# Performance work log

Hardware: AMD Instinct MI355X
Metric: run time of the kernel (lower is better)

The kernel has to match this reference:

```python
import jax, jax.numpy as jnp
import numpy as np
import math

S, B, H, NH = 2048, 1, 4096, 32
HD = H // NH          # 128 head dim
ROT = HD // 2         # 64 rotary dim per half (position_encoding_2d)


def _rotary_tables(seq_len):
    inv_freq = 1.0 / (10000.0 ** (jnp.arange(0, ROT, 2, dtype=jnp.float32) / ROT))  # [ROT/2]
    t = jnp.arange(seq_len, dtype=jnp.float32)
    freqs = jnp.einsum('i,j->ij', t, inv_freq)          # [S, ROT/2]
    emb = jnp.concatenate([freqs, freqs], axis=-1)       # [S, ROT]
    return jnp.cos(emb), jnp.sin(emb)


def _rotate_half(x):
    half = x.shape[-1] // 2
    return jnp.concatenate([-x[..., half:], x[..., :half]], axis=-1)


def _apply_rotary(q, k, cos, sin, pos):
    # q,k: [s,b,nh,ROT]; pos: [s,b]
    c = cos[pos][:, :, None, :]   # [s,b,1,ROT]
    s_ = sin[pos][:, :, None, :]
    return q * c + _rotate_half(q) * s_, k * c + _rotate_half(k) * s_


def reference(hidden_states, position_ids, attention_mask, layer_id, w_qkv, b_qkv, w_dense, b_dense):
    s, b, _ = hidden_states.shape
    # fused QKV projection (Linear: x @ W.T + b)
    qkv = jnp.einsum('sbh,oh->sbo', hidden_states, w_qkv) + b_qkv     # [s,b,3H]
    qkv = qkv.reshape(s, b, NH, 3 * HD)
    q, k, v = jnp.split(qkv, 3, axis=-1)                               # each [s,b,nh,HD]
    # 2D rotary: split head dim in two halves, rotate with pos / block pos ids
    cos, sin = _rotary_tables(s)
    pos = position_ids[:, 0, :].T        # [s,b]
    blk = position_ids[:, 1, :].T        # [s,b]
    q1, q2 = jnp.split(q, 2, axis=-1)
    k1, k2 = jnp.split(k, 2, axis=-1)
    q1, k1 = _apply_rotary(q1, k1, cos, sin, pos)
    q2, k2 = _apply_rotary(q2, k2, cos, sin, blk)
    q = jnp.concatenate([q1, q2], axis=-1)
    k = jnp.concatenate([k1, k2], axis=-1)
    # layer-id-dependent scaling (GLM numerics): q scaled down by coeff, logits scaled back up
    coeff = float(layer_id + 1)
    q = q / (math.sqrt(HD) * coeff)
    scores = jnp.einsum('sbnd,tbnd->bnst', q, k)                       # [b,nh,s,s]
    scores = jnp.where(attention_mask, jnp.asarray(-10000.0, scores.dtype), scores)
    probs = jax.nn.softmax(scores.astype(jnp.float32) * coeff, axis=-1).astype(scores.dtype)
    ctx = jnp.einsum('bnst,tbnd->sbnd', probs, v).reshape(s, b, H)     # [s,b,H]
    return jnp.einsum('sbh,oh->sbo', ctx, w_dense) + b_dense


def setup_inputs() -> dict:
    key = jax.random.key(0)
    k1, k2, k3, k4, k5, k6 = jax.random.split(key, 6)
    init = 0.02
    hidden_states = jax.random.normal(k1, (S, B, H), dtype=jnp.float32)
    # GLM-style 2D position ids: [B, 2, S] (row 0: positions, row 1: block positions)
    pos = jnp.broadcast_to(jnp.arange(S, dtype=jnp.int64), (B, S))
    blk = jnp.broadcast_to(jnp.arange(S, dtype=jnp.int64), (B, S))
    position_ids = jnp.stack([pos, blk], axis=1)                        # [B,2,S]
    # causal mask: True = masked (future positions)
    causal = jnp.triu(jnp.ones((S, S), dtype=bool), k=1)
    attention_mask = jnp.broadcast_to(causal[None, None], (B, 1, S, S))
    return {
        'hidden_states': hidden_states,
        'position_ids': position_ids,
        'attention_mask': attention_mask,
        'layer_id': 5,
        'w_qkv': jax.random.normal(k2, (3 * H, H), dtype=jnp.float32) * init,
        'b_qkv': jax.random.normal(k3, (3 * H,), dtype=jnp.float32) * init,
        'w_dense': jax.random.normal(k4, (H, H), dtype=jnp.float32) * init,
        'b_dense': jax.random.normal(k5, (H,), dtype=jnp.float32) * init,
    }
```

## Files before the change

### kernel.cpp

```cpp
#include <hip/hip_runtime.h>
#include <math.h>
#include <stdint.h>

constexpr int S  = 2048;
constexpr int H  = 4096;
constexpr int NH = 32;
constexpr int HD = 128;
constexpr int H3 = 3 * H;

typedef unsigned short u16;
typedef __bf16 bf16x8 __attribute__((ext_vector_type(8)));
typedef float  f32x4  __attribute__((ext_vector_type(4)));
typedef unsigned short us8 __attribute__((ext_vector_type(8)));

__device__ __forceinline__ u16 f2bf(float f) {
  uint32_t u = __float_as_uint(f);
  uint32_t r = (u + 0x7fff + ((u >> 16) & 1)) >> 16;
  return (u16)r;
}
__device__ __forceinline__ float bf2f(u16 u) {
  return __uint_as_float((uint32_t)u << 16);
}

__device__ __forceinline__ void load_lds16(const void* g, void* l) {
  __builtin_amdgcn_global_load_lds(
      (__attribute__((address_space(1))) void*)(uintptr_t)g,
      (__attribute__((address_space(3))) void*)l,
      16, 0, 0);
}

#define SBAR0 __builtin_amdgcn_sched_barrier(0)

__global__ __launch_bounds__(256)
void cast_all(const float* __restrict__ w_qkv, const float* __restrict__ hidden,
              const float* __restrict__ w_dense, u16* __restrict__ wq,
              u16* __restrict__ hb, u16* __restrict__ wd) {
  constexpr int NQ  = H3 * H / 4;
  constexpr int NHd = S * H / 4;
  constexpr int ND  = H * H / 4;
  constexpr int NT  = NQ + NHd + ND;
  for (int i = blockIdx.x * 256 + threadIdx.x; i < NT; i += gridDim.x * 256) {
    const float4* src;
    ushort4* dst;
    int j = i;
    if (j < NQ)            { src = (const float4*)w_qkv;  dst = (ushort4*)wq; }
    else if (j < NQ + NHd) { j -= NQ; src = (const float4*)hidden; dst = (ushort4*)hb; }
    else                   { j -= NQ + NHd; src = (const float4*)w_dense; dst = (ushort4*)wd; }
    float4 v = src[j];
    ushort4 o;
    o.x = f2bf(v.x); o.y = f2bf(v.y); o.z = f2bf(v.z); o.w = f2bf(v.w);
    dst[j] = o;
  }
}

template<int STRIDE, int OUT_BF16>
__global__ __launch_bounds__(512, 2)
void gemm256(const u16* __restrict__ A, const u16* __restrict__ W,
             const float* __restrict__ bias, void* __restrict__ Cout) {
  constexpr int K   = 4096;
  constexpr int NT  = K / 64;
  constexpr int NTM = 8;
  constexpr int TB  = 65536;
  __shared__ __attribute__((aligned(16))) unsigned char lds[2 * TB];
  const int tid = threadIdx.x, wave = tid >> 6, lane = tid & 63;
  const int l15 = lane & 15, l4 = lane >> 4;
  const int wr = wave >> 2, wc = wave & 3;

  const int nwg = gridDim.x, bid = blockIdx.x;
  const int cpx = nwg >> 3;
  const int swz = (bid & 7) * cpx + (bid >> 3);
  const int bx = swz / NTM, by = swz - bx * NTM;
  const int bm = by * 256, bn = bx * 256;

  const int srow = lane >> 3;
  const int sck  = ((lane & 7) ^ srow) * 8;
  const u16* Abase = A + (size_t)(bm + srow) * K + sck;
  const u16* Wbase = W + (size_t)(bn + srow) * K + sck;

  auto stageU = [&](int tt, int u) {
    const int b = tt & 1;
    if (u < 4) {
      const int rb = u * 64 + wave * 8;
      load_lds16(Abase + (size_t)rb * K + tt * 64, &lds[b * TB + rb * 128]);
    } else {
      const int rb = (u - 4) * 64 + wave * 8;
      load_lds16(Wbase + (size_t)rb * K + tt * 64,
                 &lds[b * TB + 32768 + rb * 128]);
    }
  };

  f32x4 acc[8][4];
#pragma unroll
  for (int i = 0; i < 8; ++i)
#pragma unroll
    for (int j = 0; j < 4; ++j) acc[i][j] = (f32x4)0.f;

#pragma unroll
  for (int u = 0; u < 8; ++u) stageU(0, u);
#pragma unroll
  for (int u = 0; u < 8; ++u) stageU(1, u);
  asm volatile("s_waitcnt vmcnt(8)" ::: "memory");
  SBAR0;
  __builtin_amdgcn_s_barrier();

  const int arow = wr * 128 + l15;
  const int brow = wc * 64 + l15;
  const int ckx  = l15 & 7;

  bf16x8 af[4][2], bfA[2][2], bfB[2][2];

  for (int t = 0; t < NT; ++t) {
    const int b0 = (t & 1) * TB;
    const bool st = (t + 2 < NT);
#pragma unroll
    for (int mi = 0; mi < 4; ++mi)
#pragma unroll
      for (int ks = 0; ks < 2; ++ks)
        af[mi][ks] = *(const bf16x8*)&lds[b0 + (arow + mi * 16) * 128 +
                                          (((ks * 4 + l4) ^ ckx) * 16)];
#pragma unroll
    for (int ni = 0; ni < 2; ++ni)
#pragma unroll
      for (int ks = 0; ks < 2; ++ks)
        bfA[ni][ks] = *(const bf16x8*)&lds[b0 + 32768 + (brow + ni * 16) * 128 +
                                           (((ks * 4 + l4) ^ ckx) * 16)];
    SBAR0; __builtin_amdgcn_s_barrier();
    asm volatile("s_waitcnt lgkmcnt(0)" ::: "memory");
    SBAR0;
    __builtin_amdgcn_s_setprio(1);
#pragma unroll
    for (int ks = 0; ks < 2; ++ks)
#pragma unroll
      for (int mi = 0; mi < 4; ++mi)
#pragma unroll
        for (int ni = 0; ni < 2; ++ni)
          acc[mi][ni] = __builtin_amdgcn_mfma_f32_16x16x32_bf16(af[mi][ks], bfA[ni][ks], acc[mi][ni], 0, 0, 0);
    __builtin_amdgcn_s_setprio(0);
    SBAR0; __builtin_amdgcn_s_barrier();
#pragma unroll
    for (int ni = 0; ni < 2; ++ni)
#pragma unroll
      for (int ks = 0; ks < 2; ++ks)
        bfB[ni][ks] = *(const bf16x8*)&lds[b0 + 32768 + (brow + (ni + 2) * 16) * 128 +
                                           (((ks * 4 + l4) ^ ckx) * 16)];
    if (st) { stageU(t + 2, 0); stageU(t + 2, 2); }
    SBAR0; __builtin_amdgcn_s_barrier();
    asm volatile("s_waitcnt lgkmcnt(0)" ::: "memory");
    SBAR0;
    __builtin_amdgcn_s_setprio(1);
#pragma unroll
    for (int ks = 0; ks < 2; ++ks)
#pragma unroll
      for (int mi = 0; mi < 4; ++mi)
#pragma unroll
        for (int ni = 0; ni < 2; ++ni)
          acc[mi][ni + 2] = __builtin_amdgcn_mfma_f32_16x16x32_bf16(af[mi][ks], bfB[ni][ks], acc[mi][ni + 2], 0, 0, 0);
    __builtin_amdgcn_s_setprio(0);
    SBAR0; __builtin_amdgcn_s_barrier();
#pragma unroll
    for (int mi = 0; mi < 4; ++mi)
#pragma unroll
      for (int ks = 0; ks < 2; ++ks)
        af[mi][ks] = *(const bf16x8*)&lds[b0 + (arow + (mi + 4) * 16) * 128 +
                                          (((ks * 4 + l4) ^ ckx) * 16)];
    if (st) { stageU(t + 2, 4); stageU(t + 2, 5); }
    SBAR0; __builtin_amdgcn_s_barrier();
    asm volatile("s_waitcnt lgkmcnt(0)" ::: "memory");
    SBAR0;
    __builtin_amdgcn_s_setprio(1);
#pragma unroll
    for (int ks = 0; ks < 2; ++ks)
#pragma unroll
      for (int mi = 0; mi < 4; ++mi)
#pragma unroll
        for (int ni = 0; ni < 2; ++ni)
          acc[mi + 4][ni] = __builtin_amdgcn_mfma_f32_16x16x32_bf16(af[mi][ks], bfA[ni][ks], acc[mi + 4][ni], 0, 0, 0);
    __builtin_amdgcn_s_setprio(0);
    SBAR0; __builtin_amdgcn_s_barrier();
    if (st) { stageU(t + 2, 1); stageU(t + 2, 3); stageU(t + 2, 6); stageU(t + 2, 7); }
    SBAR0;
    __builtin_amdgcn_s_setprio(1);
#pragma unroll
    for (int ks = 0; ks < 2; ++ks)
#pragma unroll
      for (int mi = 0; mi < 4; ++mi)
#pragma unroll
        for (int ni = 0; ni < 2; ++ni)
          acc[mi + 4][ni + 2] = __builtin_amdgcn_mfma_f32_16x16x32_bf16(af[mi][ks], bfB[ni][ks], acc[mi + 4][ni + 2], 0, 0, 0);
    __builtin_amdgcn_s_setprio(0);
    if (t < NT - 2)       asm volatile("s_waitcnt vmcnt(8)" ::: "memory");
    else if (t == NT - 2) asm volatile("s_waitcnt vmcnt(0)" ::: "memory");
    SBAR0;
    if (t < NT - 1) __builtin_amdgcn_s_barrier();
  }

#pragma unroll
  for (int ni = 0; ni < 4; ++ni) {
    const int col = bn + wc * 64 + ni * 16 + l15;
    const float bv = bias[col];
#pragma unroll
    for (int mi = 0; mi < 8; ++mi) {
#pragma unroll
      for (int r = 0; r < 4; ++r) {
        const int row = bm + wr * 128 + mi * 16 + l4 * 4 + r;
        const float v = acc[mi][ni][r] + bv;
        if (OUT_BF16) ((u16*)Cout)[(size_t)row * STRIDE + col] = f2bf(v);
        else          ((float*)Cout)[(size_t)row * STRIDE + col] = v;
      }
    }
  }
}

template<int STRIDE, int OUT_BF16>
__global__ __launch_bounds__(512, 2)
void gemm8p(const u16* __restrict__ A, const u16* __restrict__ W,
            const float* __restrict__ bias, void* __restrict__ Cout) {
  constexpr int K  = 4096;
  constexpr int NT = K / 64;
  constexpr int NTM = 16;
  constexpr int TB = 49152;
  __shared__ __attribute__((aligned(16))) unsigned char lds[3 * TB];
  const int tid = threadIdx.x, wave = tid >> 6, lane = tid & 63;
  const int l15 = lane & 15, l4 = lane >> 4;
  const int wr = wave >> 2, wc = wave & 3;

  const int nwg = gridDim.x, bid = blockIdx.x;
  const int cpx = nwg >> 3;
  const int swz = (bid & 7) * cpx + (bid >> 3);
  const int bx = swz / NTM, by = swz - bx * NTM;
  const int bm = by * 128, bn = bx * 256;

  const int srow = lane >> 3;
  const int sck  = ((lane & 7) ^ srow) * 8;
  const u16* Abase = A + (size_t)(bm + srow) * K + sck;
  const u16* Wbase = W + (size_t)(bn + srow) * K + sck;

  auto stageA = [&](int tt, int b) {
#pragma unroll
    for (int j = 0; j < 2; ++j) {
      const int rb = j * 64 + wave * 8;
      load_lds16(Abase + (size_t)rb * K + tt * 64, &lds[b * TB + rb * 128]);
    }
  };
  auto stageB = [&](int tt, int b, int u) {
#pragma unroll
    for (int j = 0; j < 2; ++j) {
      const int rb = u * 128 + j * 64 + wave * 8;
      load_lds16(Wbase + (size_t)rb * K + tt * 64,
                 &lds[b * TB + 16384 + rb * 128]);
    }
  };

  f32x4 acc[4][4];
#pragma unroll
  for (int i = 0; i < 4; ++i)
#pragma unroll
    for (int j = 0; j < 4; ++j) acc[i][j] = (f32x4)0.f;

  stageA(0, 0); stageB(0, 0, 0); stageB(0, 0, 1);
  stageA(1, 1); stageB(1, 1, 0); stageB(1, 1, 1);
  asm volatile("s_waitcnt vmcnt(6)" ::: "memory");
  SBAR0;
  __builtin_amdgcn_s_barrier();

  const int arow = wr * 64 + l15;
  const int brow = wc * 64 + l15;
  const int ckx  = l15 & 7;

  bf16x8 af[4][2], bf[4][2];

  int br = 0, bs = 2;
  for (int t = 0; t < NT; ++t) {
    const int b0 = br * TB;
#pragma unroll
    for (int mi = 0; mi < 2; ++mi)
#pragma unroll
      for (int ks = 0; ks < 2; ++ks)
        af[mi][ks] = *(const bf16x8*)&lds[b0 + (arow + mi * 16) * 128 +
                                          (((ks * 4 + l4) ^ ckx) * 16)];
#pragma unroll
    for (int ni = 0; ni < 2; ++ni)
#pragma unroll
      for (int ks = 0; ks < 2; ++ks)
        bf[ni][ks] = *(const bf16x8*)&lds[b0 + 16384 + (brow + ni * 16) * 128 +
                                          (((ks * 4 + l4) ^ ckx) * 16)];
    if (t < NT - 2) stageA(t + 2, bs);
    SBAR0; __builtin_amdgcn_s_barrier();
    asm volatile("s_waitcnt lgkmcnt(0)" ::: "memory");
    SBAR0;
    __builtin_amdgcn_s_setprio(1);
#pragma unroll
    for (int ks = 0; ks < 2; ++ks)
#pragma unroll
      for (int mi = 0; mi < 2; ++mi)
#pragma unroll
        for (int ni = 0; ni < 2; ++ni)
          acc[mi][ni] = __builtin_amdgcn_mfma_f32_16x16x32_bf16(af[mi][ks], bf[ni][ks], acc[mi][ni], 0, 0, 0);
    __builtin_amdgcn_s_setprio(0);
    SBAR0; __builtin_amdgcn_s_barrier();
#pragma unroll
    for (int ni = 2; ni < 4; ++ni)
#pragma unroll
      for (int ks = 0; ks < 2; ++ks)
        bf[ni][ks] = *(const bf16x8*)&lds[b0 + 16384 + (brow + ni * 16) * 128 +
                                          (((ks * 4 + l4) ^ ckx) * 16)];
    if (t < NT - 2) stageB(t + 2, bs, 0);
    SBAR0; __builtin_amdgcn_s_barrier();
    asm volatile("s_waitcnt lgkmcnt(0)" ::: "memory");
    SBAR0;
    __builtin_amdgcn_s_setprio(1);
#pragma unroll
    for (int ks = 0; ks < 2; ++ks)
#pragma unroll
      for (int mi = 0; mi < 2; ++mi)
#pragma unroll
        for (int ni = 2; ni < 4; ++ni)
          acc[mi][ni] = __builtin_amdgcn_mfma_f32_16x16x32_bf16(af[mi][ks], bf[ni][ks], acc[mi][ni], 0, 0, 0);
    __builtin_amdgcn_s_setprio(0);
    SBAR0; __builtin_amdgcn_s_barrier();
#pragma unroll
    for (int mi = 2; mi < 4; ++mi)
#pragma unroll
      for (int ks = 0; ks < 2; ++ks)
        af[mi][ks] = *(const bf16x8*)&lds[b0 + (arow + mi * 16) * 128 +
                                          (((ks * 4 + l4) ^ ckx) * 16)];
    if (t < NT - 2) stageB(t + 2, bs, 1);
    SBAR0; __builtin_amdgcn_s_barrier();
    asm volatile("s_waitcnt lgkmcnt(0)" ::: "memory");
    SBAR0;
    __builtin_amdgcn_s_setprio(1);
#pragma unroll
    for (int ks = 0; ks < 2; ++ks)
#pragma unroll
      for (int mi = 2; mi < 4; ++mi)
#pragma unroll
        for (int ni = 0; ni < 2; ++ni)
          acc[mi][ni] = __builtin_amdgcn_mfma_f32_16x16x32_bf16(af[mi][ks], bf[ni][ks], acc[mi][ni], 0, 0, 0);
    __builtin_amdgcn_s_setprio(0);
    SBAR0; __builtin_amdgcn_s_barrier();
    __builtin_amdgcn_s_setprio(1);
#pragma unroll
    for (int ks = 0; ks < 2; ++ks)
#pragma unroll
      for (int mi = 2; mi < 4; ++mi)
#pragma unroll
        for (int ni = 2; ni < 4; ++ni)
          acc[mi][ni] = __builtin_amdgcn_mfma_f32_16x16x32_bf16(af[mi][ks], bf[ni][ks], acc[mi][ni], 0, 0, 0);
    __builtin_amdgcn_s_setprio(0);
    if (t < NT - 1) {
      if (t < NT - 2) asm volatile("s_waitcnt vmcnt(6)" ::: "memory");
      else            asm volatile("s_waitcnt vmcnt(0)" ::: "memory");
      SBAR0;
      __builtin_amdgcn_s_barrier();
    }
    br = (br == 2) ? 0 : br + 1;
    bs = (bs == 2) ? 0 : bs + 1;
  }

#pragma unroll
  for (int ni = 0; ni < 4; ++ni) {
    const int col = bn + wc * 64 + ni * 16 + l15;
    const float bv = bias[col];
#pragma unroll
    for (int mi = 0; mi < 4; ++mi) {
#pragma unroll
      for (int r = 0; r < 4; ++r) {
        const int row = bm + wr * 64 + mi * 16 + l4 * 4 + r;
        const float v = acc[mi][ni][r] + bv;
        if (OUT_BF16) ((u16*)Cout)[(size_t)row * STRIDE + col] = f2bf(v);
        else          ((float*)Cout)[(size_t)row * STRIDE + col] = v;
      }
    }
  }
}

__global__ __launch_bounds__(256)
void rotary_fused(const u16* __restrict__ qkv,
                  u16* __restrict__ Qb, u16* __restrict__ Kb,
                  u16* __restrict__ Vt) {
  __shared__ u16 vt[64][136];
  __shared__ float2 cs_tab[64][32];
  const int s0 = blockIdx.x * 64, h = blockIdx.y;
  const int tid = threadIdx.x;

  for (int idx = tid; idx < 2048; idx += 256) {
    const int r = idx >> 5, j = idx & 31;
    const float invf = exp2f(-(float)j * (13.287712379549449f / 32.f));
    float sn, c;
    sincosf((float)(s0 + r) * invf, &sn, &c);
    cs_tab[r][j] = make_float2(c, sn);
  }
  for (int idx = tid; idx < 1024; idx += 256) {
    const int r = idx >> 4, ck = idx & 15;
    us8 v = *(const us8*)(qkv + (size_t)(s0 + r) * H3 + h * 384 + 256 + ck * 8);
    *(us8*)&vt[r][ck * 8] = v;
  }
  __syncthreads();

  for (int idx = tid; idx < 2048; idx += 256) {
    const int r  = idx >> 5;
    const int sub = idx & 31;
    const int tq = sub >> 4;
    const int ck = sub & 15;
    const int s = s0 + r;
    const u16* base = qkv + (size_t)s * H3 + h * 384 + tq * 128;
    us8 v = *(const us8*)(base + ck * 8);
    us8 p = *(const us8*)(base + ((ck * 8) ^ 32));
    const int d0 = ck * 8;
    const float sign = ((d0 & 63) < 32) ? -1.f : 1.f;
    const float sc = tq ? 1.f : 0.12751721769218683f;
    us8 o;
#pragma unroll
    for (int e = 0; e < 8; ++e) {
      const float2 cs = cs_tab[r][(d0 + e) & 31];
      o[e] = f2bf((bf2f(v[e]) * cs.x + sign * bf2f(p[e]) * cs.y) * sc);
    }
    *(us8*)((tq ? Kb : Qb) + ((size_t)h * S + s) * HD + d0) = o;
  }
  for (int idx = tid; idx < 1024; idx += 256) {
    const int d = idx >> 3, c8 = idx & 7;
    us8 o;
#pragma unroll
    for (int e = 0; e < 8; ++e) o[e] = vt[c8 * 8 + e][d];
    *(us8*)(Vt + ((size_t)h * HD + d) * S + s0 + c8 * 8) = o;
  }
}

__global__ __launch_bounds__(256)
void attn(const u16* __restrict__ Qb, const u16* __restrict__ Kb,
          const u16* __restrict__ Vt, u16* __restrict__ ctx) {
  __shared__ __attribute__((aligned(16))) unsigned char sK[2][64 * 256];
  __shared__ __attribute__((aligned(16))) unsigned char sV[2][128 * 128];
  __shared__ __attribute__((aligned(16))) unsigned char sP[4][16 * 128];
  const int bid = blockIdx.x;
  const int ixd = bid >> 3;
  const int h   = (bid & 7) * 4 + (ixd >> 5);
  const int qb  = 31 - (ixd & 31);
  const int tid = threadIdx.x, wave = tid >> 6, lane = tid & 63;
  const int l15 = lane & 15, l4 = lane >> 4;
  const int qw0 = qb * 64 + wave * 16;

  auto stage = [&](int it) {
    const int t0 = it * 64, b = it & 1;
#pragma unroll
    for (int c = 0; c < 4; ++c) {
      const int rbase = c * 16 + wave * 4;
      const int rr = rbase + (lane >> 4);
      const int p = lane & 15;
      load_lds16(Kb + ((size_t)h * S + t0 + rr) * HD + ((p ^ (rr & 15)) * 8),
                 &sK[b][rbase * 256]);
    }
#pragma unroll
    for (int c = 0; c < 4; ++c) {
      const int rbase = c * 32 + wave * 8;
      const int rr = rbase + (lane >> 3);
      const int p = lane & 7;
      load_lds16(Vt + ((size_t)h * HD + rr) * S + t0 + ((p ^ (rr & 7)) * 8),
                 &sV[b][rbase * 128]);
    }
  };

  bf16x8 qf[4];
  {
    const u16* qrow = Qb + ((size_t)h * S + qw0 + l15) * HD;
#pragma unroll
    for (int ks = 0; ks < 4; ++ks)
      qf[ks] = *(const bf16x8*)(qrow + ks * 32 + l4 * 8);
  }

  f32x4 of[8];
#pragma unroll
  for (int i = 0; i < 8; ++i) of[i] = (f32x4)0.f;
  float mrun[4] = {-1e30f, -1e30f, -1e30f, -1e30f};
  float lrun[4] = {0.f, 0.f, 0.f, 0.f};

  const int nt = qb + 1;
  stage(0);
  for (int it = 0; it < nt; ++it) {
    const int t0 = it * 64, b = it & 1;
    if (it + 1 < nt) {
      stage(it + 1);
      asm volatile("s_waitcnt vmcnt(8)" ::: "memory");
    } else {
      asm volatile("s_waitcnt vmcnt(0)" ::: "memory");
    }
    SBAR0;
    __builtin_amdgcn_s_barrier();
    SBAR0;

    f32x4 sc[4];
#pragma unroll
    for (int nf = 0; nf < 4; ++nf) sc[nf] = (f32x4)0.f;
#pragma unroll
    for (int nf = 0; nf < 4; ++nf) {
      const int trow = nf * 16 + l15;
#pragma unroll
      for (int ks = 0; ks < 4; ++ks) {
        const int chunk = ks * 4 + l4;
        bf16x8 kf = *(const bf16x8*)&sK[b][trow * 256 + ((chunk ^ (trow & 15)) * 16)];
        sc[nf] = __builtin_amdgcn_mfma_f32_16x16x32_bf16(qf[ks], kf, sc[nf], 0, 0, 0);
      }
    }

    if (it == qb) {
#pragma unroll
      for (int nf = 0; nf < 4; ++nf) {
        const int tg = t0 + nf * 16 + l15;
#pragma unroll
        for (int r = 0; r < 4; ++r) {
          const int sg = qw0 + l4 * 4 + r;
          if (tg > sg) sc[nf][r] = -1e30f;
        }
      }
    }

    f32x4 vm = sc[0];
#pragma unroll
    for (int nf = 1; nf < 4; ++nf)
#pragma unroll
      for (int r = 0; r < 4; ++r) vm[r] = fmaxf(vm[r], sc[nf][r]);
#pragma unroll
    for (int m = 1; m <= 8; m <<= 1)
#pragma unroll
      for (int r = 0; r < 4; ++r) vm[r] = fmaxf(vm[r], __shfl_xor(vm[r], m, 64));

    bool need = false;
#pragma unroll
    for (int r = 0; r < 4; ++r) need = need || (vm[r] > mrun[r] + 8.f);
    if (__builtin_amdgcn_ballot_w64(need)) {
#pragma unroll
      for (int r = 0; r < 4; ++r) {
        const float nm = fmaxf(mrun[r], vm[r]);
        const float scale = exp2f(mrun[r] - nm);
        mrun[r] = nm;
        lrun[r] *= scale;
#pragma unroll
        for (int i = 0; i < 8; ++i) of[i][r] *= scale;
      }
    }

    f32x4 rs = (f32x4)0.f;
#pragma unroll
    for (int nf = 0; nf < 4; ++nf) {
#pragma unroll
      for (int r = 0; r < 4; ++r) {
        const float p = exp2f(sc[nf][r] - mrun[r]);
        rs[r] += p;
        const int row = l4 * 4 + r;
        const int t = nf * 16 + l15;
        const int chunk = t >> 3;
        *(u16*)&sP[wave][row * 128 + ((chunk ^ (row & 7)) * 16) + (t & 7) * 2] = f2bf(p);
      }
    }
#pragma unroll
    for (int m = 1; m <= 8; m <<= 1)
#pragma unroll
      for (int r = 0; r < 4; ++r) rs[r] += __shfl_xor(rs[r], m, 64);
#pragma unroll
    for (int r = 0; r < 4; ++r) lrun[r] += rs[r];

    asm volatile("s_waitcnt lgkmcnt(0)" ::: "memory");
    SBAR0;

    bf16x8 pa[2];
#pragma unroll
    for (int ksP = 0; ksP < 2; ++ksP) {
      const int chunk = ksP * 4 + l4;
      pa[ksP] = *(const bf16x8*)&sP[wave][l15 * 128 + ((chunk ^ (l15 & 7)) * 16)];
    }
#pragma unroll
    for (int nf2 = 0; nf2 < 8; ++nf2) {
      const int d = nf2 * 16 + l15;
#pragma unroll
      for (int ksP = 0; ksP < 2; ++ksP) {
        const int chunk = ksP * 4 + l4;
        bf16x8 vf = *(const bf16x8*)&sV[b][d * 128 + ((chunk ^ (d & 7)) * 16)];
        of[nf2] = __builtin_amdgcn_mfma_f32_16x16x32_bf16(pa[ksP], vf, of[nf2], 0, 0, 0);
      }
    }
    SBAR0;
    __builtin_amdgcn_s_barrier();
  }

  float invr[4];
#pragma unroll
  for (int r = 0; r < 4; ++r) invr[r] = 1.f / lrun[r];
#pragma unroll
  for (int nf2 = 0; nf2 < 8; ++nf2) {
    const int d = nf2 * 16 + l15;
#pragma unroll
    for (int r = 0; r < 4; ++r) {
      const int srow = qw0 + l4 * 4 + r;
      ctx[(size_t)srow * H + h * HD + d] = f2bf(of[nf2][r] * invr[r]);
    }
  }
}

extern "C" void kernel_launch(void* const* d_in, const int* in_sizes, int n_in,
                              void* d_out, int out_size, void* d_ws, size_t ws_size,
                              hipStream_t stream) {
  (void)in_sizes; (void)n_in; (void)out_size; (void)ws_size;
  const float* hidden  = (const float*)d_in[0];
  const float* w_qkv   = (const float*)d_in[4];
  const float* b_qkv   = (const float*)d_in[5];
  const float* w_dense = (const float*)d_in[6];
  const float* b_dense = (const float*)d_in[7];
  float* out = (float*)d_out;

  char* ws = (char*)d_ws;
  u16* wqkvb   = (u16*)(ws + 0);
  u16* ctxb    = (u16*)(ws + 41943040);
  u16* hb      = (u16*)(ws + 100663296);
  u16* qkvb    = (u16*)(ws + 117440512);
  u16* Qbp     = (u16*)(ws + 167772160);
  u16* Kbp     = (u16*)(ws + 184549376);
  u16* Vtp     = (u16*)(ws + 201326592);
  u16* wdenseb = (u16*)(ws + 218103808);

  cast_all<<<2048, 256, 0, stream>>>(w_qkv, hidden, w_dense, wqkvb, hb, wdenseb);
  gemm256<H3, 1><<<dim3(256), 512, 0, stream>>>(hb, wqkvb, b_qkv, qkvb);
  gemm8p<H3, 1><<<dim3(256), 512, 0, stream>>>(
      hb, wqkvb + (size_t)8192 * 4096, b_qkv + 8192, (u16*)qkvb + 8192);
  rotary_fused<<<dim3(S / 64, NH), 256, 0, stream>>>(qkvb, Qbp, Kbp, Vtp);
  attn<<<dim3(1024), 256, 0, stream>>>(Qbp, Kbp, Vtp, ctxb);
  gemm8p<H, 0><<<dim3(256), 512, 0, stream>>>(ctxb, wdenseb, b_dense, out);
}
```

Measured before the change: 471.9 us.

## Single-buffer attention K/V tiles and interleave query-block order across CUs

The attention kernel drops K/V double buffering, halving its LDS footprint from about 72KB to 40KB so more workgroups can be resident per CU. The next tile's load is issued only after the current tile is consumed, which serialises load and compute inside a block and relies on other resident blocks to hide latency. The block-to-(head, query block) mapping also changes from a strict longest-first order to a snake pattern over groups of 8 query blocks, which spreads causal work differently across the grid.

```diff
diff --git a/kernel.cpp b/kernel.cpp
--- a/kernel.cpp
+++ b/kernel.cpp
@@ -429,34 +429,36 @@
 __global__ __launch_bounds__(256)
 void attn(const u16* __restrict__ Qb, const u16* __restrict__ Kb,
           const u16* __restrict__ Vt, u16* __restrict__ ctx) {
-  __shared__ __attribute__((aligned(16))) unsigned char sK[2][64 * 256];
-  __shared__ __attribute__((aligned(16))) unsigned char sV[2][128 * 128];
+  __shared__ __attribute__((aligned(16))) unsigned char sK[64 * 256];
+  __shared__ __attribute__((aligned(16))) unsigned char sV[128 * 128];
   __shared__ __attribute__((aligned(16))) unsigned char sP[4][16 * 128];
   const int bid = blockIdx.x;
   const int ixd = bid >> 3;
-  const int h   = (bid & 7) * 4 + (ixd >> 5);
-  const int qb  = 31 - (ixd & 31);
+  const int h   = (bid & 7) * 4 + (ixd & 3);
+  const int p   = ixd >> 2;
+  const int g   = p >> 3, a = p & 7;
+  const int qb  = 8 * g + ((g & 1) ? 7 - a : a);
   const int tid = threadIdx.x, wave = tid >> 6, lane = tid & 63;
   const int l15 = lane & 15, l4 = lane >> 4;
   const int qw0 = qb * 64 + wave * 16;
 
   auto stage = [&](int it) {
-    const int t0 = it * 64, b = it & 1;
+    const int t0 = it * 64;
 #pragma unroll
     for (int c = 0; c < 4; ++c) {
       const int rbase = c * 16 + wave * 4;
       const int rr = rbase + (lane >> 4);
-      const int p = lane & 15;
-      load_lds16(Kb + ((size_t)h * S + t0 + rr) * HD + ((p ^ (rr & 15)) * 8),
-                 &sK[b][rbase * 256]);
+      const int pp = lane & 15;
+      load_lds16(Kb + ((size_t)h * S + t0 + rr) * HD + ((pp ^ (rr & 15)) * 8),
+                 &sK[rbase * 256]);
     }
 #pragma unroll
     for (int c = 0; c < 4; ++c) {
       const int rbase = c * 32 + wave * 8;
       const int rr = rbase + (lane >> 3);
-      const int p = lane & 7;
-      load_lds16(Vt + ((size_t)h * HD + rr) * S + t0 + ((p ^ (rr & 7)) * 8),
-                 &sV[b][rbase * 128]);
+      const int pp = lane & 7;
+      load_lds16(Vt + ((size_t)h * HD + rr) * S + t0 + ((pp ^ (rr & 7)) * 8),
+                 &sV[rbase * 128]);
     }
   };
 
@@ -477,13 +479,8 @@
   const int nt = qb + 1;
   stage(0);
   for (int it = 0; it < nt; ++it) {
-    const int t0 = it * 64, b = it & 1;
-    if (it + 1 < nt) {
-      stage(it + 1);
-      asm volatile("s_waitcnt vmcnt(8)" ::: "memory");
-    } else {
-      asm volatile("s_waitcnt vmcnt(0)" ::: "memory");
-    }
+    const int t0 = it * 64;
+    asm volatile("s_waitcnt vmcnt(0)" ::: "memory");
     SBAR0;
     __builtin_amdgcn_s_barrier();
     SBAR0;
@@ -497,7 +494,7 @@
 #pragma unroll
       for (int ks = 0; ks < 4; ++ks) {
         const int chunk = ks * 4 + l4;
-        bf16x8 kf = *(const bf16x8*)&sK[b][trow * 256 + ((chunk ^ (trow & 15)) * 16)];
+        bf16x8 kf = *(const bf16x8*)&sK[trow * 256 + ((chunk ^ (trow & 15)) * 16)];
         sc[nf] = __builtin_amdgcn_mfma_f32_16x16x32_bf16(qf[ks], kf, sc[nf], 0, 0, 0);
       }
     }
@@ -544,12 +541,12 @@
     for (int nf = 0; nf < 4; ++nf) {
 #pragma unroll
       for (int r = 0; r < 4; ++r) {
-        const float p = exp2f(sc[nf][r] - mrun[r]);
-        rs[r] += p;
+        const float pv = exp2f(sc[nf][r] - mrun[r]);
+        rs[r] += pv;
         const int row = l4 * 4 + r;
         const int t = nf * 16 + l15;
         const int chunk = t >> 3;
-        *(u16*)&sP[wave][row * 128 + ((chunk ^ (row & 7)) * 16) + (t & 7) * 2] = f2bf(p);
+        *(u16*)&sP[wave][row * 128 + ((chunk ^ (row & 7)) * 16) + (t & 7) * 2] = f2bf(pv);
       }
     }
 #pragma unroll
@@ -574,12 +571,13 @@
 #pragma unroll
       for (int ksP = 0; ksP < 2; ++ksP) {
         const int chunk = ksP * 4 + l4;
-        bf16x8 vf = *(const bf16x8*)&sV[b][d * 128 + ((chunk ^ (d & 7)) * 16)];
+        bf16x8 vf = *(const bf16x8*)&sV[d * 128 + ((chunk ^ (d & 7)) * 16)];
         of[nf2] = __builtin_amdgcn_mfma_f32_16x16x32_bf16(pa[ksP], vf, of[nf2], 0, 0, 0);
       }
     }
     SBAR0;
     __builtin_amdgcn_s_barrier();
+    if (it + 1 < nt) stage(it + 1);
   }
 
   float invr[4];
```

After: 444.4 us, median of 2. 5.8% less time.
